# Kernel optimization log

Measured on AMD Instinct MI355X. Metric: run time of the kernel, lower is better.

## Reference

```python
import jax, jax.numpy as jnp
import numpy as np

NUM_NODES = 100000
NUM_REL = 237
D = 200            # entity_out_dim_1 * nheads_GAT_1 = 100*2
C = 50             # conv_out_channels
B = 8192           # batch of (h, r, t) triples


def setup_inputs() -> dict:
    key = jax.random.key(0)
    ks = jax.random.split(key, 8)
    heads = jax.random.randint(ks[0], (B, 1), 0, NUM_NODES)
    rels = jax.random.randint(ks[1], (B, 1), 0, NUM_REL)
    tails = jax.random.randint(ks[2], (B, 1), 0, NUM_NODES)
    batch_inputs = jnp.concatenate([heads, rels, tails], axis=1).astype(jnp.int64)
    return {
        "batch_inputs": batch_inputs,
        "final_entity_embeddings": jax.random.normal(ks[3], (NUM_NODES, D), jnp.float32),
        "final_relation_embeddings": jax.random.normal(ks[4], (NUM_REL, D), jnp.float32),
        "W_ent2rel": jax.random.normal(ks[5], (NUM_REL, D, D), jnp.float32) * (1.0 / np.sqrt(D)),
        "conv_w": jax.random.normal(ks[6], (C, 3), jnp.float32) * 0.5,
        "conv_b": jnp.zeros((C,), jnp.float32),
        "fc_w": jax.random.normal(ks[7], (1, C * D), jnp.float32) * (1.0 / np.sqrt(C * D)),
        "fc_b": jnp.zeros((1,), jnp.float32),
    }


def reference(batch_inputs, final_entity_embeddings, final_relation_embeddings,
              W_ent2rel, conv_w, conv_b, fc_w, fc_b):
    h_idx, r_idx, t_idx = batch_inputs[:, 0], batch_inputs[:, 1], batch_inputs[:, 2]
    src = final_entity_embeddings[h_idx]        # [B, D]
    rel = final_relation_embeddings[r_idx]      # [B, D]
    tail = final_entity_embeddings[t_idx]       # [B, D]
    W = W_ent2rel[r_idx]                        # [B, D, D] per-edge relation transform
    # bmm([B,1,D], [B,D,D]) -> [B,1,D], nonlinearity_ent2rel = tanh
    src = jnp.tanh(jnp.einsum('bd,bde->be', src, W))
    tail = jnp.tanh(jnp.einsum('bd,bde->be', tail, W))
    # ConvKB: stack triple as length-3 sequence, Conv2d kernel (1,3) over seq
    stacked = jnp.stack([src, rel, tail], axis=1)            # [B, 3, D]
    conv = jnp.einsum('bkd,ck->bcd', stacked, conv_w) + conv_b[None, :, None]
    conv = jax.nn.relu(conv)                                  # dropout p=0.0 (eval)
    flat = conv.reshape(conv.shape[0], -1)                    # [B, C*D] (C-major, matches torch view)
    out = flat @ fc_w.T + fc_b                                # [B, 1]
    return out
```

## Files before the change

kernel.cpp:

```cpp
#include <hip/hip_runtime.h>
#include <hip/hip_bf16.h>
#include <math.h>

#define DDIM 200
#define D4   50
#define CCH  50
#define NREL 237
#define MAXE 8
#define AROWS 16
#define NT   256
#define KT   7
#define KTKG 28
#define NCOLP 208
#define OSTRIDE 204
#define PACK_UNITS (NREL * KTKG * NCOLP)

typedef __attribute__((ext_vector_type(8))) short bf16x8;
typedef __attribute__((ext_vector_type(4))) float f32x4;

__device__ __forceinline__ uint f2bf(float x) {
    __hip_bfloat16 h = __float2bfloat16(x);
    return (uint)*reinterpret_cast<ushort*>(&h);
}
__device__ __forceinline__ float fast_tanh(float x) {
    const float xc = fminf(fmaxf(x, -20.f), 20.f);
    const float e  = __expf(2.f * xc);
    return 1.f - __fdividef(2.f, e + 1.f);
}

__global__ __launch_bounds__(1024) void prep_kernel(
    const float* __restrict__ W, ushort* __restrict__ Wpk, int do_pack,
    const int* __restrict__ bi, int B, int nblk,
    int* __restrict__ perm, int* __restrict__ blk_r,
    int* __restrict__ blk_start, int* __restrict__ blk_cnt,
    int* __restrict__ eidArr)
{
    __shared__ __align__(16) float Wlds[32][DDIM];
    __shared__ int hist[NREL];
    __shared__ int offs[NREL];
    __shared__ int wsum[16], wsum2[16];

    const int tid = threadIdx.x;

    if (blockIdx.x != 0) {
        if (!do_pack) return;
        const int blk = blockIdx.x - 1;
        const int r   = blk / KT;
        const int kt  = blk - r * KT;
        const int k0  = kt * 32;

        for (int i = tid; i < 32 * D4; i += 1024) {
            const int krow = i / D4;
            const int c4   = i - krow * D4;
            const int gk   = k0 + krow;
            float4 v = {0.f, 0.f, 0.f, 0.f};
            if (gk < DDIM)
                v = *(const float4*)(W + ((size_t)r * DDIM + gk) * DDIM + 4 * c4);
            *(float4*)&Wlds[krow][4 * c4] = v;
        }
        __syncthreads();

        for (int u = tid; u < 4 * NCOLP; u += 1024) {
            const int kg  = u / NCOLP;
            const int col = u - kg * NCOLP;
            uint4 pk = {0u, 0u, 0u, 0u};
            if (col < DDIM) {
                uint vv[8];
                #pragma unroll
                for (int j = 0; j < 8; ++j)
                    vv[j] = f2bf(Wlds[kg * 8 + j][col]);
                pk.x = vv[0] | (vv[1] << 16);
                pk.y = vv[2] | (vv[3] << 16);
                pk.z = vv[4] | (vv[5] << 16);
                pk.w = vv[6] | (vv[7] << 16);
            }
            const size_t unit = ((size_t)r * KTKG + kt * 4 + kg) * NCOLP + col;
            *(uint4*)&Wpk[unit * 8] = pk;
        }
        return;
    }

    const int lane = tid & 63;
    const int w    = tid >> 6;

    if (tid < NREL) hist[tid] = 0;
    __syncthreads();
    for (int i = tid; i < B; i += 1024)
        atomicAdd(&hist[bi[i * 3 + 1]], 1);
    __syncthreads();

    const int v  = (tid < NREL) ? hist[tid] : 0;
    const int v2 = (tid < NREL) ? (v + MAXE - 1) / MAXE : 0;
    int s = v, s2 = v2;
    #pragma unroll
    for (int off = 1; off < 64; off <<= 1) {
        const int u  = __shfl_up(s,  off, 64);
        const int u2 = __shfl_up(s2, off, 64);
        if (lane >= off) { s += u; s2 += u2; }
    }
    if (lane == 63) { wsum[w] = s; wsum2[w] = s2; }
    __syncthreads();
    int base = 0, base2 = 0;
    for (int i = 0; i < w; ++i) { base += wsum[i]; base2 += wsum2[i]; }
    const int my_off  = base  + s  - v;
    const int my_boff = base2 + s2 - v2;
    if (tid < NREL) offs[tid] = my_off;
    __syncthreads();

    for (int i = tid; i < nblk; i += 1024) blk_cnt[i] = 0;
    if (tid < NREL && v > 0) {
        const int nb = (v + MAXE - 1) / MAXE;
        const int cb = v / nb, ext = v - cb * nb;
        int pos = my_off;
        for (int j = 0; j < nb; ++j) {
            const int c = cb + (j < ext ? 1 : 0);
            blk_r[my_boff + j]     = tid;
            blk_start[my_boff + j] = pos;
            blk_cnt[my_boff + j]   = c;
            pos += c;
        }
    }
    __syncthreads();
    for (int i = tid; i < B; i += 1024) {
        const int pos = atomicAdd(&offs[bi[i * 3 + 1]], 1);
        perm[pos] = i;
        eidArr[2 * pos]     = bi[3 * i + 0];
        eidArr[2 * pos + 1] = bi[3 * i + 2];
    }
}

template <bool PACKED>
__global__ __launch_bounds__(NT) void spkbgat_mfma_kernel(
    const float*  __restrict__ ent,
    const float*  __restrict__ rel_emb,
    const float*  __restrict__ W,
    const ushort* __restrict__ Wpk,
    const float*  __restrict__ conv_w,
    const float*  __restrict__ conv_b,
    const float*  __restrict__ fc_w,
    const float*  __restrict__ fc_b,
    const int*    __restrict__ perm,
    const int*    __restrict__ blk_r,
    const int*    __restrict__ blk_start,
    const int*    __restrict__ blk_cnt,
    const int*    __restrict__ eidArr,
    int nblk,
    float*        __restrict__ out)
{
    __shared__ __align__(16) ushort Ash[KTKG * AROWS * 8];
    __shared__ __align__(16) float  Osh[AROWS][OSTRIDE];
    __shared__ __align__(16) float4 rl4[D4];
    __shared__ __align__(16) float  cwb[CCH][4];

    const int tid  = threadIdx.x;
    const int w    = tid >> 6;
    const int lane = tid & 63;
    const int l16  = lane & 15;
    const int kg   = lane >> 4;

    const int bid = blockIdx.x;
    const int q = nblk >> 3, rmd = nblk & 7;
    const int xcd = bid & 7, idx = bid >> 3;
    const int gidx = (xcd < rmd ? xcd * (q + 1) : rmd * (q + 1) + (xcd - rmd) * q) + idx;

    const int cnt = blk_cnt[gidx];
    if (cnt == 0) return;

    const int r     = blk_r[gidx];
    const int start = blk_start[gidx];
    const int rows  = 2 * cnt;

    if (tid < CCH) {
        cwb[tid][0] = conv_w[tid * 3 + 0];
        cwb[tid][1] = conv_w[tid * 3 + 1];
        cwb[tid][2] = conv_w[tid * 3 + 2];
        cwb[tid][3] = conv_b[tid];
    }
    if (tid < D4) rl4[tid] = ((const float4*)rel_emb)[r * D4 + tid];

    for (int u = tid; u < KTKG * AROWS; u += NT) {
        const int row  = u & (AROWS - 1);
        const int ktkg = u >> 4;
        uint4 pk = {0u, 0u, 0u, 0u};
        if (ktkg < 25 && row < rows) {
            const int eid = eidArr[2 * start + row];
            const float* xp = ent + (size_t)eid * DDIM + ktkg * 8;
            const float4 x0 = *(const float4*)xp;
            const float4 x1 = *(const float4*)(xp + 4);
            pk.x = f2bf(x0.x) | (f2bf(x0.y) << 16);
            pk.y = f2bf(x0.z) | (f2bf(x0.w) << 16);
            pk.z = f2bf(x1.x) | (f2bf(x1.y) << 16);
            pk.w = f2bf(x1.z) | (f2bf(x1.w) << 16);
        }
        *(uint4*)&Ash[u * 8] = pk;
    }
    __syncthreads();

    const int nslots = (w == 0) ? 4 : 3;
    const float*  __restrict__ Wr = W + (size_t)r * DDIM * DDIM;
    const ushort* __restrict__ Wp0 = Wpk + (size_t)r * KTKG * NCOLP * 8
                                   + ((size_t)kg * NCOLP) * 8 + (size_t)l16 * 8;

    bf16x8 a_frag[KT];
    #pragma unroll
    for (int kt = 0; kt < KT; ++kt)
        a_frag[kt] = *(const bf16x8*)&Ash[((kt * 4 + kg) * AROWS + l16) * 8];

    f32x4 acc[4];
    #pragma unroll
    for (int s = 0; s < 4; ++s) acc[s] = (f32x4){0.f, 0.f, 0.f, 0.f};

    if (PACKED) {
        bf16x8 bcur[4], bnxt[4];
        #pragma unroll
        for (int s = 0; s < 4; ++s)
            if (s < nslots)
                bcur[s] = *(const bf16x8*)(Wp0 + (size_t)(w + 4 * s) * 16 * 8);
        #pragma unroll
        for (int kt = 0; kt < KT; ++kt) {
            if (kt + 1 < KT) {
                const ushort* pn = Wp0 + (size_t)(kt + 1) * 4 * NCOLP * 8;
                #pragma unroll
                for (int s = 0; s < 4; ++s)
                    if (s < nslots)
                        bnxt[s] = *(const bf16x8*)(pn + (size_t)(w + 4 * s) * 16 * 8);
            }
            #pragma unroll
            for (int s = 0; s < 4; ++s)
                if (s < nslots)
                    acc[s] = __builtin_amdgcn_mfma_f32_16x16x32_bf16(
                        a_frag[kt], bcur[s], acc[s], 0, 0, 0);
            #pragma unroll
            for (int s = 0; s < 4; ++s)
                if (s < nslots) bcur[s] = bnxt[s];
        }
    } else {
        for (int kt = 0; kt < KT; ++kt) {
            const int k0b = (kt * 4 + kg) * 8;
            #pragma unroll
            for (int s = 0; s < 4; ++s) {
                if (s < nslots) {
                    const int col = (w + 4 * s) * 16 + l16;
                    bf16x8 bfr;
                    #pragma unroll
                    for (int j = 0; j < 8; ++j) {
                        const int k = k0b + j;
                        const float vv = (k < DDIM && col < DDIM) ? Wr[k * DDIM + col] : 0.f;
                        bfr[j] = (short)f2bf(vv);
                    }
                    acc[s] = __builtin_amdgcn_mfma_f32_16x16x32_bf16(
                        a_frag[kt], bfr, acc[s], 0, 0, 0);
                }
            }
        }
    }

    #pragma unroll
    for (int s = 0; s < 4; ++s) {
        if (s < nslots) {
            const int gcol = (w + 4 * s) * 16 + l16;
            if (gcol < DDIM) {
                #pragma unroll
                for (int v = 0; v < 4; ++v) {
                    const int grow = kg * 4 + v;
                    if (grow < rows)
                        Osh[grow][gcol] = fast_tanh(acc[s][v]);
                }
            }
        }
    }
    __syncthreads();

    float4 sa[2] = {{0,0,0,0}, {0,0,0,0}};
    if (lane < D4) {
        const float4 rv = rl4[lane];
        float4 se[2], te[2];
        #pragma unroll
        for (int s2 = 0; s2 < 2; ++s2) {
            const int e = w + 4 * s2;
            if (e < cnt) {
                se[s2] = *(const float4*)&Osh[2 * e][4 * lane];
                te[s2] = *(const float4*)&Osh[2 * e + 1][4 * lane];
            } else {
                se[s2] = (float4){0,0,0,0};
                te[s2] = (float4){0,0,0,0};
            }
        }
        for (int c = 0; c < CCH; ++c) {
            const float4 cw  = *(const float4*)&cwb[c][0];
            const float4 fc4 = ((const float4*)fc_w)[c * D4 + lane];
            #pragma unroll
            for (int s2 = 0; s2 < 2; ++s2) {
                const float v0 = fmaf(cw.x, se[s2].x, fmaf(cw.y, rv.x, fmaf(cw.z, te[s2].x, cw.w)));
                const float v1 = fmaf(cw.x, se[s2].y, fmaf(cw.y, rv.y, fmaf(cw.z, te[s2].y, cw.w)));
                const float v2 = fmaf(cw.x, se[s2].z, fmaf(cw.y, rv.z, fmaf(cw.z, te[s2].z, cw.w)));
                const float v3 = fmaf(cw.x, se[s2].w, fmaf(cw.y, rv.w, fmaf(cw.z, te[s2].w, cw.w)));
                sa[s2].x = fmaf(fmaxf(v0, 0.f), fc4.x, sa[s2].x);
                sa[s2].y = fmaf(fmaxf(v1, 0.f), fc4.y, sa[s2].y);
                sa[s2].z = fmaf(fmaxf(v2, 0.f), fc4.z, sa[s2].z);
                sa[s2].w = fmaf(fmaxf(v3, 0.f), fc4.w, sa[s2].w);
            }
        }
    }
    #pragma unroll
    for (int s2 = 0; s2 < 2; ++s2) {
        float sum = (sa[s2].x + sa[s2].y) + (sa[s2].z + sa[s2].w);
        #pragma unroll
        for (int off = 32; off; off >>= 1)
            sum += __shfl_down(sum, off, 64);
        const int e = w + 4 * s2;
        if (lane == 0 && e < cnt)
            out[perm[start + e]] = sum + fc_b[0];
    }
}

extern "C" void kernel_launch(void* const* d_in, const int* in_sizes, int n_in,
                              void* d_out, int out_size, void* d_ws, size_t ws_size,
                              hipStream_t stream) {
    const int*   bi      = (const int*)  d_in[0];
    const float* ent     = (const float*)d_in[1];
    const float* rel_emb = (const float*)d_in[2];
    const float* W       = (const float*)d_in[3];
    const float* conv_w  = (const float*)d_in[4];
    const float* conv_b  = (const float*)d_in[5];
    const float* fc_w    = (const float*)d_in[6];
    const float* fc_b    = (const float*)d_in[7];
    float*       out     = (float*)d_out;

    const int B    = in_sizes[0] / 3;
    const int nblk = NREL + (B + MAXE - 1) / MAXE;

    int* perm      = (int*)d_ws;
    int* blk_r     = perm + B;
    int* blk_start = blk_r + nblk;
    int* blk_cnt   = blk_start + nblk;
    int* eidArr    = blk_cnt + nblk;

    const size_t meta_bytes = (size_t)(3 * B + 3 * nblk) * sizeof(int);
    const size_t pk_off     = (meta_bytes + 255) & ~(size_t)255;
    const size_t need       = pk_off + (size_t)PACK_UNITS * 16;
    const bool   use_packed = (ws_size >= need);
    ushort* Wpk = (ushort*)((char*)d_ws + pk_off);

    const int prep_blocks = 1 + NREL * KT;
    prep_kernel<<<prep_blocks, 1024, 0, stream>>>(
        W, Wpk, use_packed ? 1 : 0, bi, B, nblk,
        perm, blk_r, blk_start, blk_cnt, eidArr);

    if (use_packed) {
        spkbgat_mfma_kernel<true><<<nblk, NT, 0, stream>>>(
            ent, rel_emb, W, Wpk, conv_w, conv_b, fc_w, fc_b,
            perm, blk_r, blk_start, blk_cnt, eidArr, nblk, out);
    } else {
        spkbgat_mfma_kernel<false><<<nblk, NT, 0, stream>>>(
            ent, rel_emb, W, Wpk, conv_w, conv_b, fc_w, fc_b,
            perm, blk_r, blk_start, blk_cnt, eidArr, nblk, out);
    }
}
```

Baseline: 54.21 us.

## Pin each relation range to one XCD in both pack and compute kernels

Relations are partitioned into eight contiguous ranges, one per XCD. Both the W-packing prep blocks and the main compute blocks are remapped with blockIdx&7 so that work for a given relation runs on the same XCD in both kernels. The intent is for the packed bf16 W written by prep to still sit in that XCD's L2 when the compute kernel reads it. In exchange, each XCD gets a fixed-capacity slot array, which launches extra empty blocks and can leave the XCDs unevenly loaded.

```diff
diff --git a/kernel.cpp b/kernel.cpp
--- a/kernel.cpp
+++ b/kernel.cpp
@@ -14,6 +14,8 @@
 #define NCOLP 208
 #define OSTRIDE 204
 #define PACK_UNITS (NREL * KTKG * NCOLP)
+#define RPX  30
+#define PPX  (RPX * KT)
 
 typedef __attribute__((ext_vector_type(8))) short bf16x8;
 typedef __attribute__((ext_vector_type(4))) float f32x4;
@@ -30,7 +32,7 @@
 
 __global__ __launch_bounds__(1024) void prep_kernel(
     const float* __restrict__ W, ushort* __restrict__ Wpk, int do_pack,
-    const int* __restrict__ bi, int B, int nblk,
+    const int* __restrict__ bi, int B, int capx,
     int* __restrict__ perm, int* __restrict__ blk_r,
     int* __restrict__ blk_start, int* __restrict__ blk_cnt,
     int* __restrict__ eidArr)
@@ -38,15 +40,21 @@
     __shared__ __align__(16) float Wlds[32][DDIM];
     __shared__ int hist[NREL];
     __shared__ int offs[NREL];
+    __shared__ int goff_sh[NREL];
     __shared__ int wsum[16], wsum2[16];
 
     const int tid = threadIdx.x;
 
     if (blockIdx.x != 0) {
         if (!do_pack) return;
-        const int blk = blockIdx.x - 1;
-        const int r   = blk / KT;
-        const int kt  = blk - r * KT;
+        const int xcd = blockIdx.x & 7;
+        int j = blockIdx.x >> 3;
+        if (xcd == 0) j -= 1;
+        const int rlo = (xcd * NREL) / 8;
+        const int rhi = ((xcd + 1) * NREL) / 8;
+        const int r   = rlo + j / KT;
+        const int kt  = j - (j / KT) * KT;
+        if (r >= rhi) return;
         const int k0  = kt * 32;
 
         for (int i = tid; i < 32 * D4; i += 1024) {
@@ -67,8 +75,8 @@
             if (col < DDIM) {
                 uint vv[8];
                 #pragma unroll
-                for (int j = 0; j < 8; ++j)
-                    vv[j] = f2bf(Wlds[kg * 8 + j][col]);
+                for (int jj = 0; jj < 8; ++jj)
+                    vv[jj] = f2bf(Wlds[kg * 8 + jj][col]);
                 pk.x = vv[0] | (vv[1] << 16);
                 pk.y = vv[2] | (vv[3] << 16);
                 pk.z = vv[4] | (vv[5] << 16);
@@ -104,19 +112,23 @@
     for (int i = 0; i < w; ++i) { base += wsum[i]; base2 += wsum2[i]; }
     const int my_off  = base  + s  - v;
     const int my_boff = base2 + s2 - v2;
-    if (tid < NREL) offs[tid] = my_off;
-    __syncthreads();
-
-    for (int i = tid; i < nblk; i += 1024) blk_cnt[i] = 0;
+    if (tid < NREL) { offs[tid] = my_off; goff_sh[tid] = my_boff; }
+    __syncthreads();
+
+    for (int i = tid; i < 8 * capx; i += 1024) blk_cnt[i] = 0;
     if (tid < NREL && v > 0) {
+        const int x   = (8 * tid) / NREL;
+        const int rlo = (x * NREL) / 8;
+        const int local0 = goff_sh[tid] - goff_sh[rlo];
         const int nb = (v + MAXE - 1) / MAXE;
         const int cb = v / nb, ext = v - cb * nb;
         int pos = my_off;
-        for (int j = 0; j < nb; ++j) {
-            const int c = cb + (j < ext ? 1 : 0);
-            blk_r[my_boff + j]     = tid;
-            blk_start[my_boff + j] = pos;
-            blk_cnt[my_boff + j]   = c;
+        for (int jj = 0; jj < nb; ++jj) {
+            const int c = cb + (jj < ext ? 1 : 0);
+            const int slot = x * capx + local0 + jj;
+            blk_r[slot]     = tid;
+            blk_start[slot] = pos;
+            blk_cnt[slot]   = c;
             pos += c;
         }
     }
@@ -144,7 +156,7 @@
     const int*    __restrict__ blk_start,
     const int*    __restrict__ blk_cnt,
     const int*    __restrict__ eidArr,
-    int nblk,
+    int capx,
     float*        __restrict__ out)
 {
     __shared__ __align__(16) ushort Ash[KTKG * AROWS * 8];
@@ -158,10 +170,8 @@
     const int l16  = lane & 15;
     const int kg   = lane >> 4;
 
-    const int bid = blockIdx.x;
-    const int q = nblk >> 3, rmd = nblk & 7;
-    const int xcd = bid & 7, idx = bid >> 3;
-    const int gidx = (xcd < rmd ? xcd * (q + 1) : rmd * (q + 1) + (xcd - rmd) * q) + idx;
+    const int bid  = blockIdx.x;
+    const int gidx = (bid & 7) * capx + (bid >> 3);
 
     const int cnt = blk_cnt[gidx];
     if (cnt == 0) return;
@@ -243,10 +253,10 @@
                     const int col = (w + 4 * s) * 16 + l16;
                     bf16x8 bfr;
                     #pragma unroll
-                    for (int j = 0; j < 8; ++j) {
-                        const int k = k0b + j;
+                    for (int jj = 0; jj < 8; ++jj) {
+                        const int k = k0b + jj;
                         const float vv = (k < DDIM && col < DDIM) ? Wr[k * DDIM + col] : 0.f;
-                        bfr[j] = (short)f2bf(vv);
+                        bfr[jj] = (short)f2bf(vv);
                     }
                     acc[s] = __builtin_amdgcn_mfma_f32_16x16x32_bf16(
                         a_frag[kt], bfr, acc[s], 0, 0, 0);
@@ -328,32 +338,33 @@
     float*       out     = (float*)d_out;
 
     const int B    = in_sizes[0] / 3;
-    const int nblk = NREL + (B + MAXE - 1) / MAXE;
+    const int capx = B / MAXE + RPX;
+    const int nslots = 8 * capx;
 
     int* perm      = (int*)d_ws;
     int* blk_r     = perm + B;
-    int* blk_start = blk_r + nblk;
-    int* blk_cnt   = blk_start + nblk;
-    int* eidArr    = blk_cnt + nblk;
-
-    const size_t meta_bytes = (size_t)(3 * B + 3 * nblk) * sizeof(int);
+    int* blk_start = blk_r + nslots;
+    int* blk_cnt   = blk_start + nslots;
+    int* eidArr    = blk_cnt + nslots;
+
+    const size_t meta_bytes = (size_t)(3 * B + 3 * nslots) * sizeof(int);
     const size_t pk_off     = (meta_bytes + 255) & ~(size_t)255;
     const size_t need       = pk_off + (size_t)PACK_UNITS * 16;
     const bool   use_packed = (ws_size >= need);
     ushort* Wpk = (ushort*)((char*)d_ws + pk_off);
 
-    const int prep_blocks = 1 + NREL * KT;
+    const int prep_blocks = 1 + 8 * PPX;
     prep_kernel<<<prep_blocks, 1024, 0, stream>>>(
-        W, Wpk, use_packed ? 1 : 0, bi, B, nblk,
+        W, Wpk, use_packed ? 1 : 0, bi, B, capx,
         perm, blk_r, blk_start, blk_cnt, eidArr);
 
     if (use_packed) {
-        spkbgat_mfma_kernel<true><<<nblk, NT, 0, stream>>>(
+        spkbgat_mfma_kernel<true><<<nslots, NT, 0, stream>>>(
             ent, rel_emb, W, Wpk, conv_w, conv_b, fc_w, fc_b,
-            perm, blk_r, blk_start, blk_cnt, eidArr, nblk, out);
+            perm, blk_r, blk_start, blk_cnt, eidArr, capx, out);
     } else {
-        spkbgat_mfma_kernel<false><<<nblk, NT, 0, stream>>>(
+        spkbgat_mfma_kernel<false><<<nslots, NT, 0, stream>>>(
             ent, rel_emb, W, Wpk, conv_w, conv_b, fc_w, fc_b,
-            perm, blk_r, blk_start, blk_cnt, eidArr, nblk, out);
-    }
-}
+            perm, blk_r, blk_start, blk_cnt, eidArr, capx, out);
+    }
+}
```

New measurement: 53.86 us. About the same (-0.6%).

## Drop W prepacking; stage fp32 W tiles through LDS in main kernel

Applied to the files above, without the earlier changes.

Removes the per-call pass that converted and packed every relation matrix into bf16 in workspace. The main kernel now loads 32-row fp32 tiles of the relation's W into shared memory, converts them to bf16 fragments on the fly, and reuses that LDS for the output staging. This avoids writing and re-reading a full packed copy of W. In exchange, every block rereads full fp32 W from global memory and synchronises each k-tile, with no load/compute overlap.

```diff
diff --git a/kernel.cpp b/kernel.cpp
--- a/kernel.cpp
+++ b/kernel.cpp
@@ -10,10 +10,8 @@
 #define AROWS 16
 #define NT   256
 #define KT   7
-#define KTKG 28
-#define NCOLP 208
+#define WSTR 204
 #define OSTRIDE 204
-#define PACK_UNITS (NREL * KTKG * NCOLP)
 
 typedef __attribute__((ext_vector_type(8))) short bf16x8;
 typedef __attribute__((ext_vector_type(4))) float f32x4;
@@ -28,58 +26,16 @@
     return 1.f - __fdividef(2.f, e + 1.f);
 }
 
-__global__ __launch_bounds__(1024) void prep_kernel(
-    const float* __restrict__ W, ushort* __restrict__ Wpk, int do_pack,
+__global__ __launch_bounds__(1024) void relsort_kernel(
     const int* __restrict__ bi, int B, int nblk,
     int* __restrict__ perm, int* __restrict__ blk_r,
     int* __restrict__ blk_start, int* __restrict__ blk_cnt,
     int* __restrict__ eidArr)
 {
-    __shared__ __align__(16) float Wlds[32][DDIM];
     __shared__ int hist[NREL];
     __shared__ int offs[NREL];
     __shared__ int wsum[16], wsum2[16];
-
-    const int tid = threadIdx.x;
-
-    if (blockIdx.x != 0) {
-        if (!do_pack) return;
-        const int blk = blockIdx.x - 1;
-        const int r   = blk / KT;
-        const int kt  = blk - r * KT;
-        const int k0  = kt * 32;
-
-        for (int i = tid; i < 32 * D4; i += 1024) {
-            const int krow = i / D4;
-            const int c4   = i - krow * D4;
-            const int gk   = k0 + krow;
-            float4 v = {0.f, 0.f, 0.f, 0.f};
-            if (gk < DDIM)
-                v = *(const float4*)(W + ((size_t)r * DDIM + gk) * DDIM + 4 * c4);
-            *(float4*)&Wlds[krow][4 * c4] = v;
-        }
-        __syncthreads();
-
-        for (int u = tid; u < 4 * NCOLP; u += 1024) {
-            const int kg  = u / NCOLP;
-            const int col = u - kg * NCOLP;
-            uint4 pk = {0u, 0u, 0u, 0u};
-            if (col < DDIM) {
-                uint vv[8];
-                #pragma unroll
-                for (int j = 0; j < 8; ++j)
-                    vv[j] = f2bf(Wlds[kg * 8 + j][col]);
-                pk.x = vv[0] | (vv[1] << 16);
-                pk.y = vv[2] | (vv[3] << 16);
-                pk.z = vv[4] | (vv[5] << 16);
-                pk.w = vv[6] | (vv[7] << 16);
-            }
-            const size_t unit = ((size_t)r * KTKG + kt * 4 + kg) * NCOLP + col;
-            *(uint4*)&Wpk[unit * 8] = pk;
-        }
-        return;
-    }
-
+    const int tid  = threadIdx.x;
     const int lane = tid & 63;
     const int w    = tid >> 6;
 
@@ -129,12 +85,10 @@
     }
 }
 
-template <bool PACKED>
 __global__ __launch_bounds__(NT) void spkbgat_mfma_kernel(
     const float*  __restrict__ ent,
     const float*  __restrict__ rel_emb,
     const float*  __restrict__ W,
-    const ushort* __restrict__ Wpk,
     const float*  __restrict__ conv_w,
     const float*  __restrict__ conv_b,
     const float*  __restrict__ fc_w,
@@ -147,8 +101,8 @@
     int nblk,
     float*        __restrict__ out)
 {
-    __shared__ __align__(16) ushort Ash[KTKG * AROWS * 8];
-    __shared__ __align__(16) float  Osh[AROWS][OSTRIDE];
+    __shared__ __align__(16) float  Wlds[32 * WSTR];
+    __shared__ __align__(16) ushort Ash[KT * 4 * AROWS * 8];
     __shared__ __align__(16) float4 rl4[D4];
     __shared__ __align__(16) float  cwb[CCH][4];
 
@@ -178,7 +132,7 @@
     }
     if (tid < D4) rl4[tid] = ((const float4*)rel_emb)[r * D4 + tid];
 
-    for (int u = tid; u < KTKG * AROWS; u += NT) {
+    for (int u = tid; u < KT * 4 * AROWS; u += NT) {
         const int row  = u & (AROWS - 1);
         const int ktkg = u >> 4;
         uint4 pk = {0u, 0u, 0u, 0u};
@@ -196,75 +150,62 @@
     }
     __syncthreads();
 
-    const int nslots = (w == 0) ? 4 : 3;
-    const float*  __restrict__ Wr = W + (size_t)r * DDIM * DDIM;
-    const ushort* __restrict__ Wp0 = Wpk + (size_t)r * KTKG * NCOLP * 8
-                                   + ((size_t)kg * NCOLP) * 8 + (size_t)l16 * 8;
-
     bf16x8 a_frag[KT];
     #pragma unroll
     for (int kt = 0; kt < KT; ++kt)
         a_frag[kt] = *(const bf16x8*)&Ash[((kt * 4 + kg) * AROWS + l16) * 8];
 
+    const int nsl = (w == 0) ? 4 : 3;
+    const float* __restrict__ Wr = W + (size_t)r * DDIM * DDIM;
+
     f32x4 acc[4];
     #pragma unroll
     for (int s = 0; s < 4; ++s) acc[s] = (f32x4){0.f, 0.f, 0.f, 0.f};
 
-    if (PACKED) {
-        bf16x8 bcur[4], bnxt[4];
+    for (int kt = 0; kt < KT; ++kt) {
+        const int k0 = kt * 32;
+        for (int i = tid; i < 32 * D4; i += NT) {
+            const int krow = i / D4;
+            const int c4   = i - krow * D4;
+            const int gk   = k0 + krow;
+            float4 v = {0.f, 0.f, 0.f, 0.f};
+            if (gk < DDIM)
+                v = *(const float4*)(Wr + (size_t)gk * DDIM + 4 * c4);
+            *(float4*)&Wlds[krow * WSTR + 4 * c4] = v;
+        }
+        __syncthreads();
+
         #pragma unroll
-        for (int s = 0; s < 4; ++s)
-            if (s < nslots)
-                bcur[s] = *(const bf16x8*)(Wp0 + (size_t)(w + 4 * s) * 16 * 8);
-        #pragma unroll
-        for (int kt = 0; kt < KT; ++kt) {
-            if (kt + 1 < KT) {
-                const ushort* pn = Wp0 + (size_t)(kt + 1) * 4 * NCOLP * 8;
-                #pragma unroll
-                for (int s = 0; s < 4; ++s)
-                    if (s < nslots)
-                        bnxt[s] = *(const bf16x8*)(pn + (size_t)(w + 4 * s) * 16 * 8);
-            }
-            #pragma unroll
-            for (int s = 0; s < 4; ++s)
-                if (s < nslots)
-                    acc[s] = __builtin_amdgcn_mfma_f32_16x16x32_bf16(
-                        a_frag[kt], bcur[s], acc[s], 0, 0, 0);
-            #pragma unroll
-            for (int s = 0; s < 4; ++s)
-                if (s < nslots) bcur[s] = bnxt[s];
-        }
-    } else {
-        for (int kt = 0; kt < KT; ++kt) {
-            const int k0b = (kt * 4 + kg) * 8;
-            #pragma unroll
-            for (int s = 0; s < 4; ++s) {
-                if (s < nslots) {
-                    const int col = (w + 4 * s) * 16 + l16;
-                    bf16x8 bfr;
+        for (int s = 0; s < 4; ++s) {
+            if (s < nsl) {
+                const int col = (w + 4 * s) * 16 + l16;
+                bf16x8 bfr;
+                if (col < DDIM) {
                     #pragma unroll
-                    for (int j = 0; j < 8; ++j) {
-                        const int k = k0b + j;
-                        const float vv = (k < DDIM && col < DDIM) ? Wr[k * DDIM + col] : 0.f;
-                        bfr[j] = (short)f2bf(vv);
-                    }
-                    acc[s] = __builtin_amdgcn_mfma_f32_16x16x32_bf16(
-                        a_frag[kt], bfr, acc[s], 0, 0, 0);
+                    for (int j = 0; j < 8; ++j)
+                        bfr[j] = (short)f2bf(Wlds[(kg * 8 + j) * WSTR + col]);
+                } else {
+                    #pragma unroll
+                    for (int j = 0; j < 8; ++j) bfr[j] = 0;
                 }
-            }
-        }
-    }
-
+                acc[s] = __builtin_amdgcn_mfma_f32_16x16x32_bf16(
+                    a_frag[kt], bfr, acc[s], 0, 0, 0);
+            }
+        }
+        __syncthreads();
+    }
+
+    float* Osh = Wlds;
     #pragma unroll
     for (int s = 0; s < 4; ++s) {
-        if (s < nslots) {
+        if (s < nsl) {
             const int gcol = (w + 4 * s) * 16 + l16;
             if (gcol < DDIM) {
                 #pragma unroll
                 for (int v = 0; v < 4; ++v) {
                     const int grow = kg * 4 + v;
                     if (grow < rows)
-                        Osh[grow][gcol] = fast_tanh(acc[s][v]);
+                        Osh[grow * OSTRIDE + gcol] = fast_tanh(acc[s][v]);
                 }
             }
         }
@@ -279,8 +220,8 @@
         for (int s2 = 0; s2 < 2; ++s2) {
             const int e = w + 4 * s2;
             if (e < cnt) {
-                se[s2] = *(const float4*)&Osh[2 * e][4 * lane];
-                te[s2] = *(const float4*)&Osh[2 * e + 1][4 * lane];
+                se[s2] = *(const float4*)&Osh[(2 * e) * OSTRIDE + 4 * lane];
+                te[s2] = *(const float4*)&Osh[(2 * e + 1) * OSTRIDE + 4 * lane];
             } else {
                 se[s2] = (float4){0,0,0,0};
                 te[s2] = (float4){0,0,0,0};
@@ -336,24 +277,10 @@
     int* blk_cnt   = blk_start + nblk;
     int* eidArr    = blk_cnt + nblk;
 
-    const size_t meta_bytes = (size_t)(3 * B + 3 * nblk) * sizeof(int);
-    const size_t pk_off     = (meta_bytes + 255) & ~(size_t)255;
-    const size_t need       = pk_off + (size_t)PACK_UNITS * 16;
-    const bool   use_packed = (ws_size >= need);
-    ushort* Wpk = (ushort*)((char*)d_ws + pk_off);
-
-    const int prep_blocks = 1 + NREL * KT;
-    prep_kernel<<<prep_blocks, 1024, 0, stream>>>(
-        W, Wpk, use_packed ? 1 : 0, bi, B, nblk,
-        perm, blk_r, blk_start, blk_cnt, eidArr);
-
-    if (use_packed) {
-        spkbgat_mfma_kernel<true><<<nblk, NT, 0, stream>>>(
-            ent, rel_emb, W, Wpk, conv_w, conv_b, fc_w, fc_b,
-            perm, blk_r, blk_start, blk_cnt, eidArr, nblk, out);
-    } else {
-        spkbgat_mfma_kernel<false><<<nblk, NT, 0, stream>>>(
-            ent, rel_emb, W, Wpk, conv_w, conv_b, fc_w, fc_b,
-            perm, blk_r, blk_start, blk_cnt, eidArr, nblk, out);
-    }
-}
+    relsort_kernel<<<1, 1024, 0, stream>>>(
+        bi, B, nblk, perm, blk_r, blk_start, blk_cnt, eidArr);
+
+    spkbgat_mfma_kernel<<<nblk, NT, 0, stream>>>(
+        ent, rel_emb, W, conv_w, conv_b, fc_w, fc_b,
+        perm, blk_r, blk_start, blk_cnt, eidArr, nblk, out);
+}
```

After: 115.5 us. 2.13x slower.
